# Optimization experiments

Hardware: AMD Instinct MI355X
Metric: run time of the kernel (lower is better)

Reference implementation:

```python
import jax, jax.numpy as jnp
import numpy as np

D, H, HD, L, F, V, R, C = 512, 8, 64, 12, 2048, 2048, 1024, 64
B, T, M = 8, 1024, 128


def posenc(t, d):
    pos = jnp.arange(t, dtype=jnp.float32)[:, None]
    div = jnp.exp(jnp.arange(0, d, 2, dtype=jnp.float32) * (-np.log(10000.0) / d))
    pe = jnp.zeros((t, d), jnp.float32)
    pe = pe.at[:, 0::2].set(jnp.sin(pos * div))
    pe = pe.at[:, 1::2].set(jnp.cos(pos * div))
    return pe


def setup_inputs():
    key = jax.random.key(0)
    ks = iter(jax.random.split(key, 32))
    s = 0.02
    x = jax.random.randint(next(ks), (B, T), 1, V)  # avoid padding_idx=0 rows
    chord_positions = jax.random.randint(next(ks), (B, M), 0, T)
    n = lambda shape: jax.random.normal(next(ks), shape, jnp.float32) * s
    emb = n((V, D)).at[0].set(0.0)  # padding_idx row zeroed
    return {
        'x': x, 'chord_positions': chord_positions, 'emb': emb,
        'rel_emb': n((L, 2 * R + 1, HD)),
        'Wq': n((L, D, D)), 'bq': jnp.zeros((L, D)),
        'Wk': n((L, D, D)), 'bk': jnp.zeros((L, D)),
        'Wv': n((L, D, D)), 'bv': jnp.zeros((L, D)),
        'Wo': n((L, D, D)), 'bo': jnp.zeros((L, D)),
        'ln1_s': jnp.ones((L, D)), 'ln1_b': jnp.zeros((L, D)),
        'W1': n((L, D, F)), 'b1': jnp.zeros((L, F)),
        'W2': n((L, F, D)), 'b2': jnp.zeros((L, D)),
        'ln2_s': jnp.ones((L, D)), 'ln2_b': jnp.zeros((L, D)),
        'Wout': n((D, V)), 'bout': jnp.zeros((V,)),
        'Wc': n((D, C)), 'bc': jnp.zeros((C,)),
    }


def _ln(z, s, b):
    mu = jnp.mean(z, -1, keepdims=True)
    var = jnp.var(z, -1, keepdims=True)
    return (z - mu) * jax.lax.rsqrt(var + 1e-5) * s + b


def _forward(x, chord_positions, emb, rel_emb, Wq, bq, Wk, bk, Wv, bv, Wo, bo,
             ln1_s, ln1_b, W1, b1, W2, b2, ln2_s, ln2_b, Wout, bout, Wc, bc):
    Bx, Tx = x.shape
    h = emb[x] * jnp.sqrt(jnp.float32(D)) + posenc(Tx, D)[None]
    pad = (x == 0)  # key padding mask
    causal = jnp.triu(jnp.ones((Tx, Tx), bool), 1)
    mask = causal[None, None] | pad[:, None, None, :]  # (B,1|H,T,T)
    rel_idx = jnp.clip(jnp.arange(Tx)[None, :] - jnp.arange(Tx)[:, None], -R, R) + R  # (T,T)
    for i in range(L):
        q = (h @ Wq[i] + bq[i]).reshape(Bx, Tx, H, HD).transpose(0, 2, 1, 3)
        k = (h @ Wk[i] + bk[i]).reshape(Bx, Tx, H, HD).transpose(0, 2, 1, 3)
        v = (h @ Wv[i] + bv[i]).reshape(Bx, Tx, H, HD).transpose(0, 2, 1, 3)
        scores = jnp.einsum('bhqd,bhkd->bhqk', q, k)
        relp = jnp.einsum('bhqd,rd->bhqr', q, rel_emb[i])  # (B,H,T,2R+1)
        scores = scores + jnp.take_along_axis(relp, rel_idx[None, None], axis=-1)
        scores = scores * (1.0 / np.sqrt(HD))
        scores = jnp.where(mask, -1e9, scores)
        a = jax.nn.softmax(scores, axis=-1)
        o = jnp.einsum('bhqk,bhkd->bhqd', a, v).transpose(0, 2, 1, 3).reshape(Bx, Tx, D)
        h = _ln(h + o @ Wo[i] + bo[i], ln1_s[i], ln1_b[i])
        f = jax.nn.relu(h @ W1[i] + b1[i]) @ W2[i] + b2[i]
        h = _ln(h + f, ln2_s[i], ln2_b[i])
    logits = h @ Wout + bout
    safe_pos = jnp.maximum(chord_positions, 0)
    gathered = h[jnp.arange(Bx)[:, None], safe_pos]  # (B,M,D)
    chord_logits = gathered @ Wc + bc
    return logits, chord_logits


def reference(x, chord_positions, emb, rel_emb, Wq, bq, Wk, bk, Wv, bv, Wo, bo,
              ln1_s, ln1_b, W1, b1, W2, b2, ln2_s, ln2_b, Wout, bout, Wc, bc):
    return _forward(x, chord_positions, emb, rel_emb, Wq, bq, Wk, bk, Wv, bv, Wo, bo,
                    ln1_s, ln1_b, W1, b1, W2, b2, ln2_s, ln2_b, Wout, bout, Wc, bc)
```

## Files before the change

kernel.cpp:

```cpp
#include <hip/hip_runtime.h>
#include <hip/hip_bf16.h>
#include <cstddef>

constexpr int B_ = 8, TT = 1024, H_ = 8, HD_ = 64, D_ = 512, F_ = 2048;
constexpr int L_ = 12, R_ = 1024, NR_ = 2049, C_ = 64, M_ = 128, V_ = 2048;
constexpr int BT_ = B_ * TT;

typedef short bf16x8_t __attribute__((ext_vector_type(8)));
typedef float f32x4_t __attribute__((ext_vector_type(4)));
typedef unsigned short ushort_t;

__device__ __forceinline__ float b2f(unsigned int u16) {
  return __uint_as_float(u16 << 16);
}
__device__ __forceinline__ ushort_t f2b(float f) {
  __hip_bfloat16 h = __float2bfloat16(f);
  return *reinterpret_cast<ushort_t*>(&h);
}
__device__ __forceinline__ void gl_lds16(const ushort_t* g, ushort_t* l) {
  __builtin_amdgcn_global_load_lds(
      (const __attribute__((address_space(1))) unsigned int*)g,
      (__attribute__((address_space(3))) unsigned int*)l, 16, 0, 0);
}

__global__ __launch_bounds__(256) void transpose_bf16_b(const float* __restrict__ src,
                                                        ushort_t* __restrict__ dst,
                                                        int K, int N,
                                                        size_t sstride, size_t dstride) {
  __shared__ float t[32][33];
  src += (size_t)blockIdx.z * sstride;
  dst += (size_t)blockIdx.z * dstride;
  int k0 = blockIdx.y * 32, n0 = blockIdx.x * 32;
  int r = threadIdx.x >> 3, c4 = (threadIdx.x & 7) * 4;
  float4 vv = *(const float4*)(src + (size_t)(k0 + r) * N + n0 + c4);
  t[r][c4] = vv.x; t[r][c4 + 1] = vv.y; t[r][c4 + 2] = vv.z; t[r][c4 + 3] = vv.w;
  __syncthreads();
  ushort4 w;
  w.x = f2b(t[c4 + 0][r]); w.y = f2b(t[c4 + 1][r]);
  w.z = f2b(t[c4 + 2][r]); w.w = f2b(t[c4 + 3][r]);
  *(ushort4*)(dst + (size_t)(n0 + r) * K + k0 + c4) = w;
}

__global__ __launch_bounds__(256) void rel_convert(const float* __restrict__ rel,
                                                   ushort_t* __restrict__ rel_bf) {
  size_t idx = ((size_t)blockIdx.x * 256 + threadIdx.x) * 4;
  const size_t total = (size_t)L_ * NR_ * HD_;
  if (idx >= total) return;
  float4 f = *(const float4*)(rel + idx);
  ushort4 w;
  w.x = f2b(f.x); w.y = f2b(f.y); w.z = f2b(f.z); w.w = f2b(f.w);
  *(ushort4*)(rel_bf + idx) = w;
}

__global__ __launch_bounds__(256) void pack_bias(const float* __restrict__ bq,
                                                 const float* __restrict__ bk,
                                                 const float* __restrict__ bv,
                                                 float* __restrict__ bqkv) {
  int idx = blockIdx.x * 256 + threadIdx.x;
  if (idx >= L_ * 1536) return;
  int l = idx / 1536, c = idx - l * 1536;
  float v;
  if (c < 512) v = bq[l * 512 + c];
  else if (c < 1024) v = bk[l * 512 + (c - 512)];
  else v = bv[l * 512 + (c - 1024)];
  bqkv[idx] = v;
}

__global__ void embed_kernel(const int* __restrict__ x, const float* __restrict__ emb,
                             float* __restrict__ h, ushort_t* __restrict__ h_bf) {
  int bt = blockIdx.x;
  int t = bt & (TT - 1);
  int tok = x[bt];
  const float c = -9.210340371976184f / 512.0f;
  size_t base = (size_t)bt * D_;
  size_t ebase = (size_t)tok * D_;
  for (int d = threadIdx.x; d < D_; d += 256) {
    int i = d >> 1;
    float div = expf((float)(2 * i) * c);
    float arg = (float)t * div;
    float pe = (d & 1) ? cosf(arg) : sinf(arg);
    float vv = emb[ebase + d] * 22.627416997969522f + pe;
    h[base + d] = vv;
    h_bf[base + d] = f2b(vv);
  }
}

template <int OUT_BF16, int RELU>
__global__ __launch_bounds__(256) void gemm_mfma(const ushort_t* __restrict__ A,
                                                 const ushort_t* __restrict__ Bt,
                                                 const float* __restrict__ bias,
                                                 void* __restrict__ Cout,
                                                 int Mm, int N, int K) {
  __shared__ ushort_t As[2][128 * 32];
  __shared__ ushort_t Bs[2][128 * 32];
  int tid = threadIdx.x;
  int m0 = blockIdx.y * 128, n0 = blockIdx.x * 128;
  int lane = tid & 63, wid = tid >> 6;
  int wr = wid >> 1, wc = wid & 1;

  f32x4_t acc[4][4];
#pragma unroll
  for (int mi = 0; mi < 4; ++mi)
#pragma unroll
    for (int ni = 0; ni < 4; ++ni) acc[mi][ni] = (f32x4_t){0.f, 0.f, 0.f, 0.f};

  int ar0 = tid >> 2, ap0 = tid & 3, akg0 = ap0 ^ ((ar0 >> 1) & 3);
  int ar1 = ar0 + 64, akg1 = ap0 ^ ((ar1 >> 1) & 3);
  const ushort_t* sA0 = A + (size_t)(m0 + ar0) * K + akg0 * 8;
  const ushort_t* sA1 = A + (size_t)(m0 + ar1) * K + akg1 * 8;
  const ushort_t* sB0 = Bt + (size_t)(n0 + ar0) * K + akg0 * 8;
  const ushort_t* sB1 = Bt + (size_t)(n0 + ar1) * K + akg1 * 8;
  int lo8 = tid * 8;

  gl_lds16(sA0, &As[0][lo8]);
  gl_lds16(sA1, &As[0][lo8 + 2048]);
  gl_lds16(sB0, &Bs[0][lo8]);
  gl_lds16(sB1, &Bs[0][lo8 + 2048]);

  int NT = K >> 5;
  int kg = lane >> 4, rl = lane & 15;
  int buf = 0;
  for (int kt = 0; kt < NT; ++kt) {
    __syncthreads();
    if (kt + 1 < NT) {
      int ko = (kt + 1) << 5;
      gl_lds16(sA0 + ko, &As[buf ^ 1][lo8]);
      gl_lds16(sA1 + ko, &As[buf ^ 1][lo8 + 2048]);
      gl_lds16(sB0 + ko, &Bs[buf ^ 1][lo8]);
      gl_lds16(sB1 + ko, &Bs[buf ^ 1][lo8 + 2048]);
    }
    bf16x8_t fa[4], fb[4];
#pragma unroll
    for (int mi = 0; mi < 4; ++mi) {
      int r = wr * 64 + mi * 16 + rl;
      fa[mi] = *(bf16x8_t*)&As[buf][r * 32 + ((kg ^ ((r >> 1) & 3)) << 3)];
    }
#pragma unroll
    for (int ni = 0; ni < 4; ++ni) {
      int r = wc * 64 + ni * 16 + rl;
      fb[ni] = *(bf16x8_t*)&Bs[buf][r * 32 + ((kg ^ ((r >> 1) & 3)) << 3)];
    }
#pragma unroll
    for (int mi = 0; mi < 4; ++mi)
#pragma unroll
      for (int ni = 0; ni < 4; ++ni)
        acc[mi][ni] = __builtin_amdgcn_mfma_f32_16x16x32_bf16(fa[mi], fb[ni], acc[mi][ni], 0, 0, 0);
    buf ^= 1;
  }

  int rg = lane >> 4;
#pragma unroll
  for (int ni = 0; ni < 4; ++ni) {
    int col = n0 + wc * 64 + ni * 16 + rl;
    float bv = bias[col];
#pragma unroll
    for (int mi = 0; mi < 4; ++mi) {
      int row0 = m0 + wr * 64 + mi * 16 + rg * 4;
#pragma unroll
      for (int r = 0; r < 4; ++r) {
        float vv = acc[mi][ni][r] + bv;
        if (RELU) vv = fmaxf(vv, 0.0f);
        if (OUT_BF16)
          ((ushort_t*)Cout)[(size_t)(row0 + r) * N + col] = f2b(vv);
        else
          ((float*)Cout)[(size_t)(row0 + r) * N + col] = vv;
      }
    }
  }
}

__global__ __launch_bounds__(256) void chord_mfma(const ushort_t* __restrict__ h_bf,
                                                  const int* __restrict__ pos,
                                                  const ushort_t* __restrict__ wcT,
                                                  const float* __restrict__ bc,
                                                  float* __restrict__ out) {
  __shared__ ushort_t As[64 * 32];
  __shared__ ushort_t Bs[64 * 32];
  int tid = threadIdx.x;
  int lane = tid & 63, w = tid >> 6;
  int rl = lane & 15, kg = lane >> 4;
  int m0 = blockIdx.x * 64;
  int ar = tid >> 2, ap = tid & 3, akg = ap ^ ((ar >> 1) & 3);
  int grow = m0 + ar;
  int b = grow >> 7;
  int p = pos[grow];
  if (p < 0) p = 0;
  const ushort_t* asrc = h_bf + ((size_t)(b * TT + p)) * D_ + akg * 8;
  const ushort_t* bsrc = wcT + (size_t)ar * D_ + akg * 8;

  f32x4_t acc[4];
#pragma unroll
  for (int ni = 0; ni < 4; ++ni) acc[ni] = (f32x4_t){0.f, 0.f, 0.f, 0.f};

  for (int kt = 0; kt < 16; ++kt) {
    uint4 va = *(const uint4*)(asrc + kt * 32);
    uint4 vb = *(const uint4*)(bsrc + kt * 32);
    __syncthreads();
    *(uint4*)&As[ar * 32 + ap * 8] = va;
    *(uint4*)&Bs[ar * 32 + ap * 8] = vb;
    __syncthreads();
    int r = 16 * w + rl;
    bf16x8_t fa = *(bf16x8_t*)&As[r * 32 + ((kg ^ ((r >> 1) & 3)) << 3)];
#pragma unroll
    for (int ni = 0; ni < 4; ++ni) {
      int rr = ni * 16 + rl;
      bf16x8_t fb = *(bf16x8_t*)&Bs[rr * 32 + ((kg ^ ((rr >> 1) & 3)) << 3)];
      acc[ni] = __builtin_amdgcn_mfma_f32_16x16x32_bf16(fa, fb, acc[ni], 0, 0, 0);
    }
  }

  int rg = lane >> 4;
#pragma unroll
  for (int ni = 0; ni < 4; ++ni) {
    int col = ni * 16 + rl;
    float bv = bc[col];
#pragma unroll
    for (int r = 0; r < 4; ++r) {
      int row = m0 + 16 * w + rg * 4 + r;
      out[(size_t)row * C_ + col] = acc[ni][r] + bv;
    }
  }
}

__global__ __launch_bounds__(256) void attn_mfma(const ushort_t* __restrict__ qkv,
                                                 const ushort_t* __restrict__ rel_bf,
                                                 ushort_t* __restrict__ o) {
  __shared__ ushort_t QPs[64 * 64];
  __shared__ ushort_t Ks[64 * 64];
  __shared__ ushort_t Vs[64 * 64];
  __shared__ ushort_t Rl[128 * 64];

  int blk = blockIdx.x;
  int u = ((blk & 15) + 5 * ((blk >> 8) & 3)) & 15;
  int qt = (u & 1) ? ((u - 1) >> 1) : (15 - (u >> 1));
  int bh = blk >> 4;
  int hh = bh & 7, b = bh >> 3;
  int t0 = qt << 6;
  int tid = threadIdx.x;
  int lane = tid & 63, w = tid >> 6;
  int lo = lane & 15, hi = lane >> 4;

  const ushort_t* qg = qkv + ((size_t)(b * TT + t0)) * 1536 + hh * 64;
  const ushort_t* kg = qkv + ((size_t)b * TT) * 1536 + 512 + hh * 64;
  const ushort_t* vg = qkv + ((size_t)b * TT) * 1536 + 1024 + hh * 64;
  const ushort_t* relb = rel_bf + (size_t)(961 - t0) * 64;

  int row_a = tid >> 3, gg_a = tid & 7;
  int row_b = row_a + 32;

  for (int idx = tid; idx < 512; idx += 256) {
    int row = idx >> 3, gg = idx & 7;
    uint4 uu = *(const uint4*)(qg + (size_t)row * 1536 + gg * 8);
    unsigned int uw[4] = {uu.x, uu.y, uu.z, uu.w};
    unsigned int ow[4];
#pragma unroll
    for (int j = 0; j < 4; ++j) {
      float f0 = b2f(uw[j] & 0xffffu) * 0.125f;
      float f1 = b2f(uw[j] >> 16) * 0.125f;
      ow[j] = (unsigned int)f2b(f0) | ((unsigned int)f2b(f1) << 16);
    }
    *(uint4*)&QPs[row * 64 + ((gg ^ (row & 7)) << 3)] = make_uint4(ow[0], ow[1], ow[2], ow[3]);
  }
  __syncthreads();

  bf16x8_t faq0 = *(bf16x8_t*)&QPs[(16 * w + lo) * 64 + ((hi ^ (lo & 7)) << 3)];
  bf16x8_t faq1 = *(bf16x8_t*)&QPs[(16 * w + lo) * 64 + (((hi + 4) ^ (lo & 7)) << 3)];

  uint4 pk0 = *(const uint4*)(kg + (size_t)row_a * 1536 + gg_a * 8);
  uint4 pk1 = *(const uint4*)(kg + (size_t)row_b * 1536 + gg_a * 8);
  uint4 pv0 = *(const uint4*)(vg + (size_t)row_a * 1536 + gg_a * 8);
  uint4 pv1 = *(const uint4*)(vg + (size_t)row_b * 1536 + gg_a * 8);
  uint4 pr0 = *(const uint4*)(relb + (size_t)row_a * 64 + gg_a * 8);
  uint4 pr1 = *(const uint4*)(relb + (size_t)(row_a + 32) * 64 + gg_a * 8);
  uint4 pr2 = *(const uint4*)(relb + (size_t)(row_a + 64) * 64 + gg_a * 8);
  uint4 pr3 = *(const uint4*)(relb + (size_t)(row_a + 96) * 64 + gg_a * 8);

  f32x4_t acc_o[4];
#pragma unroll
  for (int nd = 0; nd < 4; ++nd) acc_o[nd] = (f32x4_t){0.f, 0.f, 0.f, 0.f};
  float mrow[4] = {-1e30f, -1e30f, -1e30f, -1e30f};
  float lrow[4] = {0.f, 0.f, 0.f, 0.f};

  int vsb = (int)(size_t)(const void*)Vs;
  int tb0 = vsb + ((2 * hi + 0) * 4) * 128 + lo * 8;
  int tb1 = vsb + ((2 * hi + 1) * 4) * 128 + lo * 8;
  int tb2 = vsb + ((2 * hi + 8) * 4) * 128 + lo * 8;
  int tb3 = vsb + ((2 * hi + 9) * 4) * 128 + lo * 8;

  int nkt = (t0 >> 6) + 1;
  for (int kt = 0; kt < nkt; ++kt) {
    __syncthreads();
    *(uint4*)&Ks[row_a * 64 + ((gg_a ^ (row_a & 7)) << 3)] = pk0;
    *(uint4*)&Ks[row_b * 64 + ((gg_a ^ (row_b & 7)) << 3)] = pk1;
    *(uint4*)&Vs[((row_a >> 2) * 4 + (gg_a >> 1)) * 64 + (row_a & 3) * 16 + (gg_a & 1) * 8] = pv0;
    *(uint4*)&Vs[((row_b >> 2) * 4 + (gg_a >> 1)) * 64 + (row_b & 3) * 16 + (gg_a & 1) * 8] = pv1;
    if (kt == 0) {
      int u0 = row_a;
      *(uint4*)&Rl[u0 * 64 + ((gg_a ^ (u0 & 7)) << 3)] = pr0;
      int u1 = row_a + 32;
      *(uint4*)&Rl[u1 * 64 + ((gg_a ^ (u1 & 7)) << 3)] = pr1;
      int u2 = row_a + 64;
      *(uint4*)&Rl[u2 * 64 + ((gg_a ^ (u2 & 7)) << 3)] = pr2;
      int u3 = row_a + 96;
      *(uint4*)&Rl[u3 * 64 + ((gg_a ^ (u3 & 7)) << 3)] = pr3;
    } else {
      int ur0 = 64 + row_a, ph0 = (ur0 + (kt << 6)) & 127;
      *(uint4*)&Rl[ph0 * 64 + ((gg_a ^ (ur0 & 7)) << 3)] = pr0;
      int ur1 = 64 + row_b, ph1 = (ur1 + (kt << 6)) & 127;
      *(uint4*)&Rl[ph1 * 64 + ((gg_a ^ (ur1 & 7)) << 3)] = pr1;
    }
    __syncthreads();
    if (kt + 1 < nkt) {
      size_t ko = (size_t)((kt + 1) << 6);
      pk0 = *(const uint4*)(kg + (ko + row_a) * 1536 + gg_a * 8);
      pk1 = *(const uint4*)(kg + (ko + row_b) * 1536 + gg_a * 8);
      pv0 = *(const uint4*)(vg + (ko + row_a) * 1536 + gg_a * 8);
      pv1 = *(const uint4*)(vg + (ko + row_b) * 1536 + gg_a * 8);
      pr0 = *(const uint4*)(relb + (ko + 64 + row_a) * 64 + gg_a * 8);
      pr1 = *(const uint4*)(relb + (ko + 64 + row_b) * 64 + gg_a * 8);
    }

    f32x4_t acc_s[4], acc_r[5];
#pragma unroll
    for (int nc = 0; nc < 4; ++nc) acc_s[nc] = (f32x4_t){0.f, 0.f, 0.f, 0.f};
#pragma unroll
    for (int pt = 0; pt < 5; ++pt) acc_r[pt] = (f32x4_t){0.f, 0.f, 0.f, 0.f};

    __builtin_amdgcn_s_setprio(1);
#pragma unroll
    for (int nc = 0; nc < 4; ++nc) {
      int row = 16 * nc + lo;
      bf16x8_t fb0 = *(bf16x8_t*)&Ks[row * 64 + ((hi ^ (lo & 7)) << 3)];
      bf16x8_t fb1 = *(bf16x8_t*)&Ks[row * 64 + (((hi + 4) ^ (lo & 7)) << 3)];
      acc_s[nc] = __builtin_amdgcn_mfma_f32_16x16x32_bf16(faq0, fb0, acc_s[nc], 0, 0, 0);
      acc_s[nc] = __builtin_amdgcn_mfma_f32_16x16x32_bf16(faq1, fb1, acc_s[nc], 0, 0, 0);
    }
#pragma unroll
    for (int pt = 0; pt < 5; ++pt) {
      int r = 16 * (3 - w + pt) + lo;
      int phys = (r + (kt << 6)) & 127;
      bf16x8_t fb0 = *(bf16x8_t*)&Rl[phys * 64 + ((hi ^ (lo & 7)) << 3)];
      bf16x8_t fb1 = *(bf16x8_t*)&Rl[phys * 64 + (((hi + 4) ^ (lo & 7)) << 3)];
      acc_r[pt] = __builtin_amdgcn_mfma_f32_16x16x32_bf16(faq0, fb0, acc_r[pt], 0, 0, 0);
      acc_r[pt] = __builtin_amdgcn_mfma_f32_16x16x32_bf16(faq1, fb1, acc_r[pt], 0, 0, 0);
    }
    __builtin_amdgcn_s_setprio(0);

    bool islast = (kt == nkt - 1);
#pragma unroll
    for (int g = 0; g < 4; ++g) {
      int rl = 4 * hi + g;
      int dd = lo + 15 - rl;
      int src = (lane & 48) | (dd & 15);
      bool carry = (dd & 16) != 0;
      float sh0 = __shfl(acc_r[0][g], src);
      float sh1 = __shfl(acc_r[1][g], src);
      float sh2 = __shfl(acc_r[2][g], src);
      float sh3 = __shfl(acc_r[3][g], src);
      float sh4 = __shfl(acc_r[4][g], src);
      float s0 = acc_s[0][g] + (carry ? sh1 : sh0);
      float s1 = acc_s[1][g] + (carry ? sh2 : sh1);
      float s2 = acc_s[2][g] + (carry ? sh3 : sh2);
      float s3 = acc_s[3][g] + (carry ? sh4 : sh3);
      if (islast) {
        int rw = 16 * w + rl;
        if (lo > rw) s0 = -1e30f;
        if (16 + lo > rw) s1 = -1e30f;
        if (32 + lo > rw) s2 = -1e30f;
        if (48 + lo > rw) s3 = -1e30f;
      }
      float mx = fmaxf(fmaxf(s0, s1), fmaxf(s2, s3));
      mx = fmaxf(mx, __shfl_xor(mx, 1));
      mx = fmaxf(mx, __shfl_xor(mx, 2));
      mx = fmaxf(mx, __shfl_xor(mx, 4));
      mx = fmaxf(mx, __shfl_xor(mx, 8));
      float mnew = fmaxf(mrow[g], mx);
      float scale = __expf(mrow[g] - mnew);
      mrow[g] = mnew;
      float p0 = __expf(s0 - mnew);
      float p1 = __expf(s1 - mnew);
      float p2 = __expf(s2 - mnew);
      float p3 = __expf(s3 - mnew);
      float ls = p0 + p1 + p2 + p3;
      ls += __shfl_xor(ls, 1);
      ls += __shfl_xor(ls, 2);
      ls += __shfl_xor(ls, 4);
      ls += __shfl_xor(ls, 8);
      lrow[g] = lrow[g] * scale + ls;
      acc_o[0][g] *= scale; acc_o[1][g] *= scale;
      acc_o[2][g] *= scale; acc_o[3][g] *= scale;
      ushort_t* pr = &QPs[(16 * w + rl) * 64];
      int rsw = rl & 7, l3 = lo >> 3, l7 = lo & 7;
      pr[(((0 + l3) ^ rsw) << 3) + l7] = f2b(p0);
      pr[(((2 + l3) ^ rsw) << 3) + l7] = f2b(p1);
      pr[(((4 + l3) ^ rsw) << 3) + l7] = f2b(p2);
      pr[(((6 + l3) ^ rsw) << 3) + l7] = f2b(p3);
    }

    bf16x8_t pa0 = *(bf16x8_t*)&QPs[(16 * w + lo) * 64 + ((hi ^ (lo & 7)) << 3)];
    bf16x8_t pa1 = *(bf16x8_t*)&QPs[(16 * w + lo) * 64 + (((hi + 4) ^ (lo & 7)) << 3)];
    unsigned long long tr0[4], tr1[4], tr2[4], tr3[4];
#pragma unroll
    for (int nd = 0; nd < 4; ++nd) {
      asm volatile("ds_read_b64_tr_b16 %0, %1" : "=v"(tr0[nd]) : "v"(tb0 + nd * 128));
      asm volatile("ds_read_b64_tr_b16 %0, %1" : "=v"(tr1[nd]) : "v"(tb1 + nd * 128));
      asm volatile("ds_read_b64_tr_b16 %0, %1" : "=v"(tr2[nd]) : "v"(tb2 + nd * 128));
      asm volatile("ds_read_b64_tr_b16 %0, %1" : "=v"(tr3[nd]) : "v"(tb3 + nd * 128));
    }
    asm volatile("s_waitcnt lgkmcnt(0)" ::: "memory");
    __builtin_amdgcn_sched_barrier(0);
    __builtin_amdgcn_s_setprio(1);
#pragma unroll
    for (int nd = 0; nd < 4; ++nd) {
      union { unsigned long long u[2]; bf16x8_t v; } cv0, cv1;
      cv0.u[0] = tr0[nd]; cv0.u[1] = tr1[nd];
      cv1.u[0] = tr2[nd]; cv1.u[1] = tr3[nd];
      acc_o[nd] = __builtin_amdgcn_mfma_f32_16x16x32_bf16(pa0, cv0.v, acc_o[nd], 0, 0, 0);
      acc_o[nd] = __builtin_amdgcn_mfma_f32_16x16x32_bf16(pa1, cv1.v, acc_o[nd], 0, 0, 0);
    }
    __builtin_amdgcn_s_setprio(0);
  }

  ushort_t* og = o + ((size_t)(b * TT + t0 + 16 * w)) * D_ + hh * HD_;
#pragma unroll
  for (int g = 0; g < 4; ++g) {
    int rl = 4 * hi + g;
    float inv = 1.0f / lrow[g];
#pragma unroll
    for (int nd = 0; nd < 4; ++nd)
      og[(size_t)rl * D_ + 16 * nd + lo] = f2b(acc_o[nd][g] * inv);
  }
}

__global__ __launch_bounds__(256) void ln_res_kernel(float* __restrict__ h,
                                                     const float* __restrict__ y,
                                                     const float* __restrict__ s,
                                                     const float* __restrict__ bvec,
                                                     ushort_t* __restrict__ h_bf) {
  int row = blockIdx.x;
  int tid = threadIdx.x;
  size_t base = (size_t)row * D_;
  float z0 = h[base + tid] + y[base + tid];
  float z1 = h[base + tid + 256] + y[base + tid + 256];
  __shared__ float r1[256], r2[256];
  r1[tid] = z0 + z1;
  r2[tid] = z0 * z0 + z1 * z1;
  __syncthreads();
  for (int off = 128; off > 0; off >>= 1) {
    if (tid < off) {
      r1[tid] += r1[tid + off];
      r2[tid] += r2[tid + off];
    }
    __syncthreads();
  }
  float mu = r1[0] * (1.0f / 512.0f);
  float var = r2[0] * (1.0f / 512.0f) - mu * mu;
  float rs = rsqrtf(var + 1e-5f);
  float o0 = (z0 - mu) * rs * s[tid] + bvec[tid];
  float o1 = (z1 - mu) * rs * s[tid + 256] + bvec[tid + 256];
  h[base + tid] = o0;
  h[base + tid + 256] = o1;
  h_bf[base + tid] = f2b(o0);
  h_bf[base + tid + 256] = f2b(o1);
}

extern "C" void kernel_launch(void* const* d_in, const int* in_sizes, int n_in,
                              void* d_out, int out_size, void* d_ws, size_t ws_size,
                              hipStream_t stream) {
  const int* x = (const int*)d_in[0];
  const int* cpos = (const int*)d_in[1];
  const float* emb = (const float*)d_in[2];
  const float* rel = (const float*)d_in[3];
  const float* Wq = (const float*)d_in[4];
  const float* bq = (const float*)d_in[5];
  const float* Wk = (const float*)d_in[6];
  const float* bk = (const float*)d_in[7];
  const float* Wv = (const float*)d_in[8];
  const float* bv = (const float*)d_in[9];
  const float* Wo = (const float*)d_in[10];
  const float* bo = (const float*)d_in[11];
  const float* ln1s = (const float*)d_in[12];
  const float* ln1b = (const float*)d_in[13];
  const float* W1 = (const float*)d_in[14];
  const float* b1 = (const float*)d_in[15];
  const float* W2 = (const float*)d_in[16];
  const float* b2 = (const float*)d_in[17];
  const float* ln2s = (const float*)d_in[18];
  const float* ln2b = (const float*)d_in[19];
  const float* Wout = (const float*)d_in[20];
  const float* bout = (const float*)d_in[21];
  const float* Wc = (const float*)d_in[22];
  const float* bc = (const float*)d_in[23];

  const size_t SZ = (size_t)BT_ * D_;
  const size_t WPROJ = (size_t)D_ * D_;
  const size_t WFFN = (size_t)D_ * F_;

  float* h = (float*)d_ws;
  float* y = h + SZ;
  ushort_t* h_bf = (ushort_t*)(y + SZ);
  ushort_t* qkv_bf = h_bf + SZ;
  ushort_t* o_bf = qkv_bf + (size_t)BT_ * 1536;
  ushort_t* mid_bf = o_bf + SZ;
  ushort_t* wqkvT = mid_bf + (size_t)BT_ * F_;
  ushort_t* woT = wqkvT + (size_t)L_ * 1536 * 512;
  ushort_t* w1T = woT + L_ * WPROJ;
  ushort_t* w2T = w1T + L_ * WFFN;
  ushort_t* woutT = w2T + L_ * WFFN;
  ushort_t* wcT = woutT + (size_t)D_ * V_;
  ushort_t* rel_bf = wcT + (size_t)D_ * C_;
  float* bqkv = (float*)(rel_bf + (size_t)L_ * NR_ * HD_);
  float* out = (float*)d_out;

  transpose_bf16_b<<<dim3(16, 16, 12), 256, 0, stream>>>(Wq, wqkvT, 512, 512, WPROJ, (size_t)1536 * 512);
  transpose_bf16_b<<<dim3(16, 16, 12), 256, 0, stream>>>(Wk, wqkvT + (size_t)512 * 512, 512, 512, WPROJ, (size_t)1536 * 512);
  transpose_bf16_b<<<dim3(16, 16, 12), 256, 0, stream>>>(Wv, wqkvT + (size_t)1024 * 512, 512, 512, WPROJ, (size_t)1536 * 512);
  transpose_bf16_b<<<dim3(16, 16, 12), 256, 0, stream>>>(Wo, woT, 512, 512, WPROJ, WPROJ);
  transpose_bf16_b<<<dim3(64, 16, 12), 256, 0, stream>>>(W1, w1T, 512, 2048, WFFN, WFFN);
  transpose_bf16_b<<<dim3(16, 64, 12), 256, 0, stream>>>(W2, w2T, 2048, 512, WFFN, WFFN);
  transpose_bf16_b<<<dim3(64, 16, 1), 256, 0, stream>>>(Wout, woutT, 512, 2048, 0, 0);
  transpose_bf16_b<<<dim3(2, 16, 1), 256, 0, stream>>>(Wc, wcT, 512, 64, 0, 0);
  rel_convert<<<1537, 256, 0, stream>>>(rel, rel_bf);
  pack_bias<<<(L_ * 1536 + 255) / 256, 256, 0, stream>>>(bq, bk, bv, bqkv);

  embed_kernel<<<BT_, 256, 0, stream>>>(x, emb, h, h_bf);

  dim3 gQKV(1536 / 128, BT_ / 128);
  dim3 gProj(D_ / 128, BT_ / 128);
  dim3 gF1(F_ / 128, BT_ / 128);
  dim3 gOut(V_ / 128, BT_ / 128);

  for (int l = 0; l < L_; ++l) {
    gemm_mfma<1, 0><<<gQKV, 256, 0, stream>>>(h_bf, wqkvT + (size_t)l * 1536 * 512,
                                              bqkv + l * 1536, qkv_bf, BT_, 1536, D_);
    attn_mfma<<<B_ * H_ * (TT / 64), 256, 0, stream>>>(qkv_bf, rel_bf + (size_t)l * NR_ * HD_, o_bf);
    gemm_mfma<0, 0><<<gProj, 256, 0, stream>>>(o_bf, woT + l * WPROJ, bo + l * D_, y, BT_, D_, D_);
    ln_res_kernel<<<BT_, 256, 0, stream>>>(h, y, ln1s + l * D_, ln1b + l * D_, h_bf);
    gemm_mfma<1, 1><<<gF1, 256, 0, stream>>>(h_bf, w1T + l * WFFN, b1 + l * F_, mid_bf, BT_, F_, D_);
    gemm_mfma<0, 0><<<gProj, 256, 0, stream>>>(mid_bf, w2T + l * WFFN, b2 + l * D_, y, BT_, D_, F_);
    ln_res_kernel<<<BT_, 256, 0, stream>>>(h, y, ln2s + l * D_, ln2b + l * D_, h_bf);
  }

  gemm_mfma<0, 0><<<gOut, 256, 0, stream>>>(h_bf, woutT, bout, out, BT_, V_, D_);
  chord_mfma<<<(B_ * M_) / 64, 256, 0, stream>>>(h_bf, cpos, wcT, bc, out + (size_t)BT_ * V_);
}
```

Measured before the change: 2.585 ms.

## Swap GEMM LDS-direct double buffering for register staging, bf16 residual output, vectorized LN/embed

The GEMM no longer uses global_load_lds into a double-buffered LDS tile. It now loads the next k-tile into registers, stores it to a single LDS buffer and synchronizes twice per step. The Wo and W2 projection outputs become bf16 instead of fp32, which halves their write and read traffic into the residual layernorm, at some cost in precision. Layernorm and embedding use vectorized float2 access, and positional encodings are precomputed once per position with fast sincos instead of per token. The GEMM change gives up the asynchronous direct-to-LDS copy and the overlap from double buffering, which could slow the dominant kernels.

New measurement: 2.395 ms. 1.08x faster.

```diff
diff --git a/kernel.cpp b/kernel.cpp
--- a/kernel.cpp
+++ b/kernel.cpp
@@ -16,11 +16,6 @@
 __device__ __forceinline__ ushort_t f2b(float f) {
   __hip_bfloat16 h = __float2bfloat16(f);
   return *reinterpret_cast<ushort_t*>(&h);
-}
-__device__ __forceinline__ void gl_lds16(const ushort_t* g, ushort_t* l) {
-  __builtin_amdgcn_global_load_lds(
-      (const __attribute__((address_space(1))) unsigned int*)g,
-      (__attribute__((address_space(3))) unsigned int*)l, 16, 0, 0);
 }
 
 __global__ __launch_bounds__(256) void transpose_bf16_b(const float* __restrict__ src,
@@ -66,23 +61,35 @@
   bqkv[idx] = v;
 }
 
-__global__ void embed_kernel(const int* __restrict__ x, const float* __restrict__ emb,
-                             float* __restrict__ h, ushort_t* __restrict__ h_bf) {
+__global__ __launch_bounds__(256) void posenc_kernel(float* __restrict__ pe) {
+  int t = blockIdx.x;
+  int i = threadIdx.x;
+  const float c = -9.210340371976184f / 512.0f;
+  float div = expf((float)(2 * i) * c);
+  float arg = (float)t * div;
+  float sv, cv;
+  __sincosf(arg, &sv, &cv);
+  *(float2*)&pe[(size_t)t * D_ + 2 * i] = make_float2(sv, cv);
+}
+
+__global__ __launch_bounds__(256) void embed_kernel(const int* __restrict__ x,
+                                                    const float* __restrict__ emb,
+                                                    const float* __restrict__ pe,
+                                                    float* __restrict__ h,
+                                                    ushort_t* __restrict__ h_bf) {
   int bt = blockIdx.x;
   int t = bt & (TT - 1);
   int tok = x[bt];
-  const float c = -9.210340371976184f / 512.0f;
   size_t base = (size_t)bt * D_;
   size_t ebase = (size_t)tok * D_;
-  for (int d = threadIdx.x; d < D_; d += 256) {
-    int i = d >> 1;
-    float div = expf((float)(2 * i) * c);
-    float arg = (float)t * div;
-    float pe = (d & 1) ? cosf(arg) : sinf(arg);
-    float vv = emb[ebase + d] * 22.627416997969522f + pe;
-    h[base + d] = vv;
-    h_bf[base + d] = f2b(vv);
-  }
+  int d = threadIdx.x * 2;
+  float2 e2 = *(const float2*)&emb[ebase + d];
+  float2 p2 = *(const float2*)&pe[(size_t)t * D_ + d];
+  float v0 = e2.x * 22.627416997969522f + p2.x;
+  float v1 = e2.y * 22.627416997969522f + p2.y;
+  *(float2*)&h[base + d] = make_float2(v0, v1);
+  unsigned int ob = (unsigned int)f2b(v0) | ((unsigned int)f2b(v1) << 16);
+  *(unsigned int*)&h_bf[base + d] = ob;
 }
 
 template <int OUT_BF16, int RELU>
@@ -91,8 +98,8 @@
                                                  const float* __restrict__ bias,
                                                  void* __restrict__ Cout,
                                                  int Mm, int N, int K) {
-  __shared__ ushort_t As[2][128 * 32];
-  __shared__ ushort_t Bs[2][128 * 32];
+  __shared__ ushort_t As[128 * 32];
+  __shared__ ushort_t Bs[128 * 32];
   int tid = threadIdx.x;
   int m0 = blockIdx.y * 128, n0 = blockIdx.x * 128;
   int lane = tid & 63, wid = tid >> 6;
@@ -104,48 +111,51 @@
 #pragma unroll
     for (int ni = 0; ni < 4; ++ni) acc[mi][ni] = (f32x4_t){0.f, 0.f, 0.f, 0.f};
 
-  int ar0 = tid >> 2, ap0 = tid & 3, akg0 = ap0 ^ ((ar0 >> 1) & 3);
-  int ar1 = ar0 + 64, akg1 = ap0 ^ ((ar1 >> 1) & 3);
-  const ushort_t* sA0 = A + (size_t)(m0 + ar0) * K + akg0 * 8;
-  const ushort_t* sA1 = A + (size_t)(m0 + ar1) * K + akg1 * 8;
-  const ushort_t* sB0 = Bt + (size_t)(n0 + ar0) * K + akg0 * 8;
-  const ushort_t* sB1 = Bt + (size_t)(n0 + ar1) * K + akg1 * 8;
-  int lo8 = tid * 8;
-
-  gl_lds16(sA0, &As[0][lo8]);
-  gl_lds16(sA1, &As[0][lo8 + 2048]);
-  gl_lds16(sB0, &Bs[0][lo8]);
-  gl_lds16(sB1, &Bs[0][lo8 + 2048]);
+  int c0 = tid, c1 = tid + 256;
+  int ar0 = c0 >> 2, ap0 = c0 & 3, akg0 = ap0 ^ ((ar0 >> 1) & 3);
+  int ar1 = c1 >> 2, ap1 = c1 & 3, akg1 = ap1 ^ ((ar1 >> 1) & 3);
+  const ushort_t* Arow0 = A + (size_t)(m0 + ar0) * K + akg0 * 8;
+  const ushort_t* Arow1 = A + (size_t)(m0 + ar1) * K + akg1 * 8;
+  const ushort_t* Brow0 = Bt + (size_t)(n0 + ar0) * K + akg0 * 8;
+  const ushort_t* Brow1 = Bt + (size_t)(n0 + ar1) * K + akg1 * 8;
+
+  uint4 ra0 = *(const uint4*)(Arow0);
+  uint4 ra1 = *(const uint4*)(Arow1);
+  uint4 rb0 = *(const uint4*)(Brow0);
+  uint4 rb1 = *(const uint4*)(Brow1);
 
   int NT = K >> 5;
   int kg = lane >> 4, rl = lane & 15;
-  int buf = 0;
   for (int kt = 0; kt < NT; ++kt) {
+    __syncthreads();
+    *(uint4*)&As[ar0 * 32 + ap0 * 8] = ra0;
+    *(uint4*)&As[ar1 * 32 + ap1 * 8] = ra1;
+    *(uint4*)&Bs[ar0 * 32 + ap0 * 8] = rb0;
+    *(uint4*)&Bs[ar1 * 32 + ap1 * 8] = rb1;
     __syncthreads();
     if (kt + 1 < NT) {
       int ko = (kt + 1) << 5;
-      gl_lds16(sA0 + ko, &As[buf ^ 1][lo8]);
-      gl_lds16(sA1 + ko, &As[buf ^ 1][lo8 + 2048]);
-      gl_lds16(sB0 + ko, &Bs[buf ^ 1][lo8]);
-      gl_lds16(sB1 + ko, &Bs[buf ^ 1][lo8 + 2048]);
+      ra0 = *(const uint4*)(Arow0 + ko);
+      ra1 = *(const uint4*)(Arow1 + ko);
+      rb0 = *(const uint4*)(Brow0 + ko);
+      rb1 = *(const uint4*)(Brow1 + ko);
     }
     bf16x8_t fa[4], fb[4];
 #pragma unroll
     for (int mi = 0; mi < 4; ++mi) {
       int r = wr * 64 + mi * 16 + rl;
-      fa[mi] = *(bf16x8_t*)&As[buf][r * 32 + ((kg ^ ((r >> 1) & 3)) << 3)];
+      fa[mi] = *(bf16x8_t*)&As[r * 32 + ((kg ^ ((r >> 1) & 3)) << 3)];
     }
 #pragma unroll
     for (int ni = 0; ni < 4; ++ni) {
       int r = wc * 64 + ni * 16 + rl;
-      fb[ni] = *(bf16x8_t*)&Bs[buf][r * 32 + ((kg ^ ((r >> 1) & 3)) << 3)];
+      fb[ni] = *(bf16x8_t*)&Bs[r * 32 + ((kg ^ ((r >> 1) & 3)) << 3)];
     }
 #pragma unroll
     for (int mi = 0; mi < 4; ++mi)
 #pragma unroll
       for (int ni = 0; ni < 4; ++ni)
         acc[mi][ni] = __builtin_amdgcn_mfma_f32_16x16x32_bf16(fa[mi], fb[ni], acc[mi][ni], 0, 0, 0);
-    buf ^= 1;
   }
 
   int rg = lane >> 4;
@@ -433,15 +443,18 @@
 }
 
 __global__ __launch_bounds__(256) void ln_res_kernel(float* __restrict__ h,
-                                                     const float* __restrict__ y,
+                                                     const ushort_t* __restrict__ y_bf,
                                                      const float* __restrict__ s,
                                                      const float* __restrict__ bvec,
                                                      ushort_t* __restrict__ h_bf) {
   int row = blockIdx.x;
   int tid = threadIdx.x;
   size_t base = (size_t)row * D_;
-  float z0 = h[base + tid] + y[base + tid];
-  float z1 = h[base + tid + 256] + y[base + tid + 256];
+  int d = tid * 2;
+  float2 h2 = *(const float2*)&h[base + d];
+  unsigned int yy = *(const unsigned int*)&y_bf[base + d];
+  float z0 = h2.x + b2f(yy & 0xffffu);
+  float z1 = h2.y + b2f(yy >> 16);
   __shared__ float r1[256], r2[256];
   r1[tid] = z0 + z1;
   r2[tid] = z0 * z0 + z1 * z1;
@@ -456,12 +469,13 @@
   float mu = r1[0] * (1.0f / 512.0f);
   float var = r2[0] * (1.0f / 512.0f) - mu * mu;
   float rs = rsqrtf(var + 1e-5f);
-  float o0 = (z0 - mu) * rs * s[tid] + bvec[tid];
-  float o1 = (z1 - mu) * rs * s[tid + 256] + bvec[tid + 256];
-  h[base + tid] = o0;
-  h[base + tid + 256] = o1;
-  h_bf[base + tid] = f2b(o0);
-  h_bf[base + tid + 256] = f2b(o1);
+  float2 s2 = *(const float2*)&s[d];
+  float2 b2 = *(const float2*)&bvec[d];
+  float o0 = (z0 - mu) * rs * s2.x + b2.x;
+  float o1 = (z1 - mu) * rs * s2.y + b2.y;
+  *(float2*)&h[base + d] = make_float2(o0, o1);
+  unsigned int ob = (unsigned int)f2b(o0) | ((unsigned int)f2b(o1) << 16);
+  *(unsigned int*)&h_bf[base + d] = ob;
 }
 
 extern "C" void kernel_launch(void* const* d_in, const int* in_sizes, int n_in,
@@ -497,8 +511,8 @@
   const size_t WFFN = (size_t)D_ * F_;
 
   float* h = (float*)d_ws;
-  float* y = h + SZ;
-  ushort_t* h_bf = (ushort_t*)(y + SZ);
+  ushort_t* y_bf = (ushort_t*)(h + SZ);
+  ushort_t* h_bf = (ushort_t*)(h + 2 * SZ);
   ushort_t* qkv_bf = h_bf + SZ;
   ushort_t* o_bf = qkv_bf + (size_t)BT_ * 1536;
   ushort_t* mid_bf = o_bf + SZ;
@@ -510,6 +524,7 @@
   ushort_t* wcT = woutT + (size_t)D_ * V_;
   ushort_t* rel_bf = wcT + (size_t)D_ * C_;
   float* bqkv = (float*)(rel_bf + (size_t)L_ * NR_ * HD_);
+  float* pe = bqkv + L_ * 1536;
   float* out = (float*)d_out;
 
   transpose_bf16_b<<<dim3(16, 16, 12), 256, 0, stream>>>(Wq, wqkvT, 512, 512, WPROJ, (size_t)1536 * 512);
@@ -522,8 +537,9 @@
   transpose_bf16_b<<<dim3(2, 16, 1), 256, 0, stream>>>(Wc, wcT, 512, 64, 0, 0);
   rel_convert<<<1537, 256, 0, stream>>>(rel, rel_bf);
   pack_bias<<<(L_ * 1536 + 255) / 256, 256, 0, stream>>>(bq, bk, bv, bqkv);
-
-  embed_kernel<<<BT_, 256, 0, stream>>>(x, emb, h, h_bf);
+  posenc_kernel<<<TT, 256, 0, stream>>>(pe);
+
+  embed_kernel<<<BT_, 256, 0, stream>>>(x, emb, pe, h, h_bf);
 
   dim3 gQKV(1536 / 128, BT_ / 128);
   dim3 gProj(D_ / 128, BT_ / 128);
@@ -534,11 +550,11 @@
     gemm_mfma<1, 0><<<gQKV, 256, 0, stream>>>(h_bf, wqkvT + (size_t)l * 1536 * 512,
                                               bqkv + l * 1536, qkv_bf, BT_, 1536, D_);
     attn_mfma<<<B_ * H_ * (TT / 64), 256, 0, stream>>>(qkv_bf, rel_bf + (size_t)l * NR_ * HD_, o_bf);
-    gemm_mfma<0, 0><<<gProj, 256, 0, stream>>>(o_bf, woT + l * WPROJ, bo + l * D_, y, BT_, D_, D_);
-    ln_res_kernel<<<BT_, 256, 0, stream>>>(h, y, ln1s + l * D_, ln1b + l * D_, h_bf);
+    gemm_mfma<1, 0><<<gProj, 256, 0, stream>>>(o_bf, woT + l * WPROJ, bo + l * D_, y_bf, BT_, D_, D_);
+    ln_res_kernel<<<BT_, 256, 0, stream>>>(h, y_bf, ln1s + l * D_, ln1b + l * D_, h_bf);
     gemm_mfma<1, 1><<<gF1, 256, 0, stream>>>(h_bf, w1T + l * WFFN, b1 + l * F_, mid_bf, BT_, F_, D_);
-    gemm_mfma<0, 0><<<gProj, 256, 0, stream>>>(mid_bf, w2T + l * WFFN, b2 + l * D_, y, BT_, D_, F_);
-    ln_res_kernel<<<BT_, 256, 0, stream>>>(h, y, ln2s + l * D_, ln2b + l * D_, h_bf);
+    gemm_mfma<1, 0><<<gProj, 256, 0, stream>>>(mid_bf, w2T + l * WFFN, b2 + l * D_, y_bf, BT_, D_, F_);
+    ln_res_kernel<<<BT_, 256, 0, stream>>>(h, y_bf, ln2s + l * D_, ln2b + l * D_, h_bf);
   }
 
   gemm_mfma<0, 0><<<gOut, 256, 0, stream>>>(h_bf, woutT, bout, out, BT_, V_, D_);
```
